# Optimization experiments

Measured on AMD Instinct MI355X. Metric: run time of the kernel, lower is better.

## Reference

```python
import jax, jax.numpy as jnp
import numpy as np

B, L, H, HS, OUT = 4, 512, 768, 64, 16  # batch, seq_len, hidden, head_size, output_size


def setup_inputs() -> dict:
    key = jax.random.key(0)
    ks = jax.random.split(key, 4)
    return {
        "x": jax.random.normal(ks[0], (B, L, H), dtype=jnp.float32),
        "Wq": jax.random.normal(ks[1], (H, HS), dtype=jnp.float32) * 0.02,
        "bq": jnp.zeros((HS,), dtype=jnp.float32),
        "Wk": jax.random.normal(ks[2], (H, HS), dtype=jnp.float32) * 0.02,
        "bk": jnp.zeros((HS,), dtype=jnp.float32),
        "Wb": jax.random.normal(ks[3], (4 * HS, OUT), dtype=jnp.float32) * 0.02,
        "bb": jnp.zeros((OUT,), dtype=jnp.float32),
    }


def _tri_indices(seq_len):
    # pair p corresponds to (start=i, end=j) with j >= i, ordered by i then j
    idx_start = np.repeat(np.arange(seq_len), np.arange(seq_len, 0, -1))
    idx_end = np.concatenate([np.arange(i, seq_len) for i in range(seq_len)])
    return idx_start, idx_end


def reference(x, Wq, bq, Wk, bk, Wb, bb):
    seq_len = x.shape[1]
    idx_start, idx_end = _tri_indices(seq_len)  # static numpy, P = L*(L+1)/2

    # Project per-token first (math-equivalent to projecting the gathered
    # pair tensors, since Linear is applied token-wise), then gather pairs.
    q = x @ Wq + bq  # [B, L, HS]
    k = x @ Wk + bk  # [B, L, HS]

    q_start = q[:, idx_start]  # query(start_token_hidden)  [B, P, HS]
    q_end = q[:, idx_end]      # query(end_token_hidden)
    k_end = k[:, idx_end]      # key(end_token_hidden) == key_start == key_end

    # entity_type_bias(cat([query_start, key_start, query_end, key_end]))
    feat = jnp.concatenate([q_start, k_end, q_end, k_end], axis=-1) @ Wb + bb  # [B, P, OUT]

    # einsum('blnh,blnh->bln') with n=1 -> per-pair dot product, broadcast over OUT
    score = jnp.einsum('bph,bph->bp', q_start, k_end)[..., None]  # [B, P, 1]
    return score + feat  # [B, P, OUT]
```

## Files before the change

### kernel.cpp

```cpp
#include <hip/hip_runtime.h>
#include <hip/hip_bf16.h>

#define Bc   4
#define Lc   512
#define Hc   768
#define HSc  64
#define OUTc 16
#define Pc   131328
#define NTOK 2048

typedef float  floatx4 __attribute__((ext_vector_type(4)));
typedef short  bf16x8  __attribute__((ext_vector_type(8)));
typedef float  f32x4   __attribute__((ext_vector_type(4)));


__device__ __forceinline__ unsigned short f2bf(float f) {
    unsigned int u = __float_as_uint(f);
    return (unsigned short)((u + 0x7FFFu + ((u >> 16) & 1u)) >> 16);
}

__global__ __launch_bounds__(256) void prep_kernel(
    const float* __restrict__ x, const float* __restrict__ Wq,
    const float* __restrict__ Wk,
    unsigned short* __restrict__ xbf, unsigned short* __restrict__ Wt)
{
    const int bx  = blockIdx.x;
    const int tid = threadIdx.x;
    if (bx < 512) {
        const float4* xg = (const float4*)x;
        const int base = bx * 768;
        #pragma unroll
        for (int i = 0; i < 3; ++i) {
            const int idx = base + tid + i * 256;
            const float4 v = xg[idx];
            ushort4 o;
            o.x = f2bf(v.x); o.y = f2bf(v.y); o.z = f2bf(v.z); o.w = f2bf(v.w);
            ((ushort4*)xbf)[idx] = o;
        }
    } else {
        const int k0 = (bx - 512) * 16;
        __shared__ unsigned short T[128][16];
        const int c  = tid & 127;
        const int kg = tid >> 7;
        const float* Wsrc = (c < 64) ? Wq : Wk;
        const int cc = c & 63;
        #pragma unroll
        for (int kk = 0; kk < 8; ++kk) {
            const int k = k0 + kg * 8 + kk;
            T[c][kg * 8 + kk] = f2bf(Wsrc[k * HSc + cc]);
        }
        __syncthreads();
        const int n = tid >> 1;
        const int h = tid & 1;
        const unsigned short* src = &T[n][h * 8];
        ushort4* dst = (ushort4*)(Wt + (size_t)n * Hc + k0 + h * 8);
        dst[0] = make_ushort4(src[0], src[1], src[2], src[3]);
        dst[1] = make_ushort4(src[4], src[5], src[6], src[7]);
    }
}

__global__ __launch_bounds__(256) void gemm_kernel(
    const unsigned short* __restrict__ xbf, const unsigned short* __restrict__ Wt,
    const float* __restrict__ bq, const float* __restrict__ bk,
    float* __restrict__ qws, float* __restrict__ kws)
{
    const int bx   = blockIdx.x;
    const int mb   = bx >> 1;
    const int nh   = bx & 1;
    const int tid  = threadIdx.x;
    const int w    = tid >> 6;
    const int lane = tid & 63;
    const int l15  = lane & 15;
    const int quad = lane >> 4;

    const int m0 = mb * 16;
    const int nb = nh * 64 + w * 16;

    const unsigned short* ap = xbf + (size_t)(m0 + l15) * Hc + quad * 8;
    const unsigned short* bp = Wt  + (size_t)(nb + l15) * Hc + quad * 8;

    f32x4 acc = {0.f, 0.f, 0.f, 0.f};
    #pragma unroll
    for (int k0 = 0; k0 < Hc; k0 += 32) {
        const bf16x8 a = *(const bf16x8*)(ap + k0);
        const bf16x8 b = *(const bf16x8*)(bp + k0);
        acc = __builtin_amdgcn_mfma_f32_16x16x32_bf16(a, b, acc, 0, 0, 0);
    }

    const int  gn   = nb + l15;
    const bool isq  = (gn < 64);
    const int  col  = gn & 63;
    const float bias = isq ? bq[col] : bk[col];
    float* dst = isq ? qws : kws;
    #pragma unroll
    for (int r = 0; r < 4; ++r) {
        const int tok = m0 + quad * 4 + r;
        dst[(size_t)tok * HSc + col] = acc[r] + bias;
    }
}

__global__ __launch_bounds__(256) void ae_kernel(
    const float* __restrict__ qws, const float* __restrict__ kws,
    const float* __restrict__ Wb, const float* __restrict__ bb,
    float* __restrict__ Aws, float* __restrict__ Ews)
{
    __shared__ float lWb[256 * OUTc];
    __shared__ float lqk[8][128];
    const int tid = threadIdx.x;
    const int tok_base = blockIdx.x * 8;
    #pragma unroll
    for (int i = 0; i < 16; ++i) lWb[tid + i * 256] = Wb[tid + i * 256];
    for (int i = tid; i < 8 * 128; i += 256) {
        const int t = i >> 7, c = i & 127;
        lqk[t][c] = (c < 64) ? qws[(size_t)(tok_base + t) * HSc + c]
                             : kws[(size_t)(tok_base + t) * HSc + (c - 64)];
    }
    __syncthreads();
    const int t = tid >> 5;
    const int c = tid & 31;
    const int tok = tok_base + t;
    const float* row = lqk[t];
    if (c < 16) {
        float a = 0.f;
        #pragma unroll 8
        for (int h = 0; h < 64; ++h) a += row[h] * lWb[h * OUTc + c];
        Aws[(size_t)tok * OUTc + c] = a;
    } else {
        const int o = c - 16;
        float ev = bb[o];
        #pragma unroll 8
        for (int h = 0; h < 64; ++h) {
            ev += row[h]      * lWb[(128 + h) * OUTc + o];
            ev += row[64 + h] * (lWb[(64 + h) * OUTc + o] + lWb[(192 + h) * OUTc + o]);
        }
        Ews[(size_t)tok * OUTc + o] = ev;
    }
}

__global__ __launch_bounds__(256) void pair_kernel(
    const float* __restrict__ qws, const float* __restrict__ kws,
    const float* __restrict__ Aws, const float* __restrict__ Ews,
    float* __restrict__ out)
{
    const int j = blockIdx.x;
    const int i = blockIdx.y;
    const int b = blockIdx.z;
    if (j < (i >> 2)) return;

    __shared__ alignas(16) float q_tile[16][64];
    __shared__ alignas(16) float A_tile[16][16];

    const int tid = threadIdx.x;
    const int s0 = i * 16;
    const int e0 = j * 64;

    {
        const int r = tid >> 4, c4 = tid & 15;
        ((float4*)q_tile[r])[c4] =
            ((const float4*)(qws + ((size_t)b * Lc + s0 + r) * HSc))[c4];
        if (tid < 64) {
            const int ra = tid >> 2, ca = tid & 3;
            ((float4*)A_tile[ra])[ca] =
                ((const float4*)(Aws + ((size_t)b * Lc + s0 + ra) * OUTc))[ca];
        }
    }
    __syncthreads();

    const int g = tid >> 2;
    const int l = tid & 3;
    const int e = e0 + g;

    const float4* kk = (const float4*)(kws + ((size_t)b * Lc + e) * HSc);
    const float4 kv0 = kk[l];
    const float4 kv1 = kk[4 + l];
    const float4 kv2 = kk[8 + l];
    const float4 kv3 = kk[12 + l];
    const float4 ev  = ((const float4*)(Ews + ((size_t)b * Lc + e) * OUTc))[l];

    float* ob = out + (size_t)b * Pc * OUTc;

    #pragma unroll 8
    for (int sl = 0; sl < 16; ++sl) {
        const int s = s0 + sl;
        const float4* qq = (const float4*)q_tile[sl];
        const float4 qv0 = qq[l];
        const float4 qv1 = qq[4 + l];
        const float4 qv2 = qq[8 + l];
        const float4 qv3 = qq[12 + l];

        float sc = qv0.x * kv0.x + qv0.y * kv0.y + qv0.z * kv0.z + qv0.w * kv0.w
                 + qv1.x * kv1.x + qv1.y * kv1.y + qv1.z * kv1.z + qv1.w * kv1.w
                 + qv2.x * kv2.x + qv2.y * kv2.y + qv2.z * kv2.z + qv2.w * kv2.w
                 + qv3.x * kv3.x + qv3.y * kv3.y + qv3.z * kv3.z + qv3.w * kv3.w;
        sc += __shfl_xor(sc, 1);
        sc += __shfl_xor(sc, 2);

        if (e >= s) {
            const float4 av = ((const float4*)A_tile[sl])[l];
            const int row = s * (2 * Lc + 1 - s) / 2 + (e - s);
            floatx4 r;
            r.x = av.x + ev.x + sc;
            r.y = av.y + ev.y + sc;
            r.z = av.z + ev.z + sc;
            r.w = av.w + ev.w + sc;
            __builtin_nontemporal_store(r, (floatx4*)(ob + (size_t)row * OUTc) + l);
        }
    }
}

extern "C" void kernel_launch(void* const* d_in, const int* in_sizes, int n_in,
                              void* d_out, int out_size, void* d_ws, size_t ws_size,
                              hipStream_t stream) {
    const float* x  = (const float*)d_in[0];
    const float* Wq = (const float*)d_in[1];
    const float* bq = (const float*)d_in[2];
    const float* Wk = (const float*)d_in[3];
    const float* bk = (const float*)d_in[4];
    const float* Wb = (const float*)d_in[5];
    const float* bb = (const float*)d_in[6];

    float* ws  = (float*)d_ws;
    float* qws = ws;
    float* kws = ws + 131072;
    float* Aws = ws + 262144;
    float* Ews = ws + 294912;
    unsigned short* xbf = (unsigned short*)(ws + 327680);
    unsigned short* Wt  = xbf + (size_t)NTOK * Hc;

    prep_kernel<<<dim3(560), dim3(256), 0, stream>>>(x, Wq, Wk, xbf, Wt);
    gemm_kernel<<<dim3(256), dim3(256), 0, stream>>>(xbf, Wt, bq, bk, qws, kws);
    ae_kernel<<<dim3(256), dim3(256), 0, stream>>>(qws, kws, Wb, bb, Aws, Ews);
    pair_kernel<<<dim3(8, 32, 4), dim3(256), 0, stream>>>(
        qws, kws, Aws, Ews, (float*)d_out);
}
```

Baseline: 100.1 us.

## Fuse prep, projection GEMM and bias-feature kernels; compact pair grid

Merges the bf16 conversion, the Q/K projection GEMM and the per-token A/E feature computation into one kernel. x is converted into a padded shared-memory tile, and Wq/Wk are read and converted on the fly per MFMA step, which removes the intermediate bf16 workspaces and two launches. The pair kernel now launches only the upper-triangular tiles by decoding a linear block index, so empty blocks are no longer scheduled. In exchange, the fused kernel has only 128 blocks and does strided, uncoalesced weight loads with conversion inside the GEMM loop, which may reduce parallelism and bandwidth efficiency.

```diff
diff --git a/kernel.cpp b/kernel.cpp
--- a/kernel.cpp
+++ b/kernel.cpp
@@ -1,5 +1,4 @@
 #include <hip/hip_runtime.h>
-#include <hip/hip_bf16.h>
 
 #define Bc   4
 #define Lc   512
@@ -8,6 +7,7 @@
 #define OUTc 16
 #define Pc   131328
 #define NTOK 2048
+#define XPITCH 776
 
 typedef float  floatx4 __attribute__((ext_vector_type(4)));
 typedef short  bf16x8  __attribute__((ext_vector_type(8)));
@@ -19,106 +19,75 @@
     return (unsigned short)((u + 0x7FFFu + ((u >> 16) & 1u)) >> 16);
 }
 
-__global__ __launch_bounds__(256) void prep_kernel(
+__global__ __launch_bounds__(512) void qkae_kernel(
     const float* __restrict__ x, const float* __restrict__ Wq,
-    const float* __restrict__ Wk,
-    unsigned short* __restrict__ xbf, unsigned short* __restrict__ Wt)
+    const float* __restrict__ Wk, const float* __restrict__ bq,
+    const float* __restrict__ bk, const float* __restrict__ Wb,
+    const float* __restrict__ bb,
+    float* __restrict__ qws, float* __restrict__ kws,
+    float* __restrict__ Aws, float* __restrict__ Ews)
 {
-    const int bx  = blockIdx.x;
-    const int tid = threadIdx.x;
-    if (bx < 512) {
-        const float4* xg = (const float4*)x;
-        const int base = bx * 768;
-        #pragma unroll
-        for (int i = 0; i < 3; ++i) {
-            const int idx = base + tid + i * 256;
-            const float4 v = xg[idx];
-            ushort4 o;
-            o.x = f2bf(v.x); o.y = f2bf(v.y); o.z = f2bf(v.z); o.w = f2bf(v.w);
-            ((ushort4*)xbf)[idx] = o;
-        }
-    } else {
-        const int k0 = (bx - 512) * 16;
-        __shared__ unsigned short T[128][16];
-        const int c  = tid & 127;
-        const int kg = tid >> 7;
-        const float* Wsrc = (c < 64) ? Wq : Wk;
-        const int cc = c & 63;
-        #pragma unroll
-        for (int kk = 0; kk < 8; ++kk) {
-            const int k = k0 + kg * 8 + kk;
-            T[c][kg * 8 + kk] = f2bf(Wsrc[k * HSc + cc]);
-        }
-        __syncthreads();
-        const int n = tid >> 1;
-        const int h = tid & 1;
-        const unsigned short* src = &T[n][h * 8];
-        ushort4* dst = (ushort4*)(Wt + (size_t)n * Hc + k0 + h * 8);
-        dst[0] = make_ushort4(src[0], src[1], src[2], src[3]);
-        dst[1] = make_ushort4(src[4], src[5], src[6], src[7]);
-    }
-}
-
-__global__ __launch_bounds__(256) void gemm_kernel(
-    const unsigned short* __restrict__ xbf, const unsigned short* __restrict__ Wt,
-    const float* __restrict__ bq, const float* __restrict__ bk,
-    float* __restrict__ qws, float* __restrict__ kws)
-{
-    const int bx   = blockIdx.x;
-    const int mb   = bx >> 1;
-    const int nh   = bx & 1;
+    __shared__ alignas(16) unsigned short xs[16 * XPITCH];
+    __shared__ float lWb[256 * OUTc];
+    __shared__ float lqk[16][128];
+
     const int tid  = threadIdx.x;
+    const int m0   = blockIdx.x * 16;
     const int w    = tid >> 6;
     const int lane = tid & 63;
     const int l15  = lane & 15;
     const int quad = lane >> 4;
-
-    const int m0 = mb * 16;
-    const int nb = nh * 64 + w * 16;
-
-    const unsigned short* ap = xbf + (size_t)(m0 + l15) * Hc + quad * 8;
-    const unsigned short* bp = Wt  + (size_t)(nb + l15) * Hc + quad * 8;
+    const bool isq = (w < 4);
+    const int  wn  = isq ? w : (w - 4);
+    const int  nq  = wn * 16 + l15;
+
+    #pragma unroll
+    for (int i = 0; i < 8; ++i) lWb[tid + i * 512] = Wb[tid + i * 512];
+
+    {
+        const float4* xg = (const float4*)(x + (size_t)m0 * Hc);
+        #pragma unroll
+        for (int i = 0; i < 6; ++i) {
+            const int idx = tid + i * 512;
+            const int r   = idx / 192;
+            const int c4  = idx - r * 192;
+            const float4 v = xg[idx];
+            *(ushort4*)(xs + r * XPITCH + c4 * 4) =
+                make_ushort4(f2bf(v.x), f2bf(v.y), f2bf(v.z), f2bf(v.w));
+        }
+    }
+    __syncthreads();
+
+    const float* bsrc = isq ? Wq : Wk;
+    const unsigned short* ap = xs + l15 * XPITCH + quad * 8;
 
     f32x4 acc = {0.f, 0.f, 0.f, 0.f};
-    #pragma unroll
+    #pragma unroll 4
     for (int k0 = 0; k0 < Hc; k0 += 32) {
-        const bf16x8 a = *(const bf16x8*)(ap + k0);
-        const bf16x8 b = *(const bf16x8*)(bp + k0);
-        acc = __builtin_amdgcn_mfma_f32_16x16x32_bf16(a, b, acc, 0, 0, 0);
-    }
-
-    const int  gn   = nb + l15;
-    const bool isq  = (gn < 64);
-    const int  col  = gn & 63;
-    const float bias = isq ? bq[col] : bk[col];
+        const bf16x8 af = *(const bf16x8*)(ap + k0);
+        const int kb = k0 + quad * 8;
+        bf16x8 bf;
+        #pragma unroll
+        for (int j = 0; j < 8; ++j)
+            bf[j] = (short)f2bf(bsrc[(kb + j) * HSc + nq]);
+        acc = __builtin_amdgcn_mfma_f32_16x16x32_bf16(af, bf, acc, 0, 0, 0);
+    }
+
+    const float bias = isq ? bq[nq] : bk[nq];
     float* dst = isq ? qws : kws;
+    const int cbase = isq ? nq : (64 + nq);
     #pragma unroll
     for (int r = 0; r < 4; ++r) {
-        const int tok = m0 + quad * 4 + r;
-        dst[(size_t)tok * HSc + col] = acc[r] + bias;
-    }
-}
-
-__global__ __launch_bounds__(256) void ae_kernel(
-    const float* __restrict__ qws, const float* __restrict__ kws,
-    const float* __restrict__ Wb, const float* __restrict__ bb,
-    float* __restrict__ Aws, float* __restrict__ Ews)
-{
-    __shared__ float lWb[256 * OUTc];
-    __shared__ float lqk[8][128];
-    const int tid = threadIdx.x;
-    const int tok_base = blockIdx.x * 8;
-    #pragma unroll
-    for (int i = 0; i < 16; ++i) lWb[tid + i * 256] = Wb[tid + i * 256];
-    for (int i = tid; i < 8 * 128; i += 256) {
-        const int t = i >> 7, c = i & 127;
-        lqk[t][c] = (c < 64) ? qws[(size_t)(tok_base + t) * HSc + c]
-                             : kws[(size_t)(tok_base + t) * HSc + (c - 64)];
+        const int t = quad * 4 + r;
+        const float v = acc[r] + bias;
+        dst[(size_t)(m0 + t) * HSc + nq] = v;
+        lqk[t][cbase] = v;
     }
     __syncthreads();
-    const int t = tid >> 5;
-    const int c = tid & 31;
-    const int tok = tok_base + t;
+
+    const int t   = tid >> 5;
+    const int c   = tid & 31;
+    const int tok = m0 + t;
     const float* row = lqk[t];
     if (c < 16) {
         float a = 0.f;
@@ -142,10 +111,14 @@
     const float* __restrict__ Aws, const float* __restrict__ Ews,
     float* __restrict__ out)
 {
-    const int j = blockIdx.x;
-    const int i = blockIdx.y;
-    const int b = blockIdx.z;
-    if (j < (i >> 2)) return;
+    int n = blockIdx.x;
+    int g = 0;
+    int cnt = 32;
+    while (n >= cnt) { n -= cnt; ++g; cnt = 4 * (8 - g); }
+    const int span = 8 - g;
+    const int i = g * 4 + n / span;
+    const int j = g + n % span;
+    const int b = blockIdx.y;
 
     __shared__ alignas(16) float q_tile[16][64];
     __shared__ alignas(16) float A_tile[16][16];
@@ -166,9 +139,9 @@
     }
     __syncthreads();
 
-    const int g = tid >> 2;
+    const int gidx = tid >> 2;
     const int l = tid & 3;
-    const int e = e0 + g;
+    const int e = e0 + gidx;
 
     const float4* kk = (const float4*)(kws + ((size_t)b * Lc + e) * HSc);
     const float4 kv0 = kk[l];
@@ -224,12 +197,9 @@
     float* kws = ws + 131072;
     float* Aws = ws + 262144;
     float* Ews = ws + 294912;
-    unsigned short* xbf = (unsigned short*)(ws + 327680);
-    unsigned short* Wt  = xbf + (size_t)NTOK * Hc;
-
-    prep_kernel<<<dim3(560), dim3(256), 0, stream>>>(x, Wq, Wk, xbf, Wt);
-    gemm_kernel<<<dim3(256), dim3(256), 0, stream>>>(xbf, Wt, bq, bk, qws, kws);
-    ae_kernel<<<dim3(256), dim3(256), 0, stream>>>(qws, kws, Wb, bb, Aws, Ews);
-    pair_kernel<<<dim3(8, 32, 4), dim3(256), 0, stream>>>(
+
+    qkae_kernel<<<dim3(128), dim3(512), 0, stream>>>(
+        x, Wq, Wk, bq, bk, Wb, bb, qws, kws, Aws, Ews);
+    pair_kernel<<<dim3(144, 4), dim3(256), 0, stream>>>(
         qws, kws, Aws, Ews, (float*)d_out);
 }
```

After: 92.06 us. 8.0% less time.
